# Kernel optimization log

Measured on AMD Instinct MI355X. Metric: run time of the kernel, lower is better.

The kernel has to match this reference:

```python
import jax, jax.numpy as jnp
import numpy as np
import math

B, S, E, H, F, V, L = 2, 2048, 1024, 16, 4096, 32000, 2
D = E // H
START = 1
EPS = 1e-6


def setup_inputs() -> dict:
    key = jax.random.key(0)
    ks = jax.random.split(key, 16)
    k_emb = 1.0 / math.sqrt(V)
    std = 0.02
    inp = {
        "tokens": jax.random.randint(ks[0], (B, S), 0, V),
        "word_embed": jax.random.normal(ks[1], (V, E), jnp.float32) * k_emb,
        "pos_embed": jax.random.normal(ks[2], (S, E), jnp.float32) * k_emb,
        "unembed_b": jnp.zeros((V,), jnp.float32),
        "kqv_w": jax.random.normal(ks[3], (L, 3 * E, E), jnp.float32) * std,
        "wo_w": jax.random.normal(ks[4], (L, E, E), jnp.float32) * std,
        "up_w": jax.random.normal(ks[5], (L, F, E), jnp.float32) * std,
        "up_b": jnp.zeros((L, F), jnp.float32),
        "down_w": jax.random.normal(ks[6], (L, E, F), jnp.float32) * std,
        "down_b": jnp.zeros((L, E), jnp.float32),
        "ln1_s": jnp.ones((L, E), jnp.float32),
        "ln1_b": jnp.zeros((L, E), jnp.float32),
        "ln2_s": jnp.ones((L, E), jnp.float32),
        "ln2_b": jnp.zeros((L, E), jnp.float32),
    }
    return inp


def _layer_norm(x, scale, bias):
    m = jnp.mean(x, axis=-1, keepdims=True)
    v = jnp.var(x, axis=-1, keepdims=True)  # biased, matches torch LayerNorm
    return (x - m) / jnp.sqrt(v + EPS) * scale + bias


def _causal_block_mask(tokens):
    # block-diagonal segments split at START tokens, plus causal triu
    is_start = tokens == START
    seg = jnp.cumsum(is_start, axis=1)  # [B,S]
    block = seg[:, :, None] != seg[:, None, :]  # [B,S,S]
    triu = jnp.triu(jnp.ones((S, S), bool), k=1)
    return triu[None, :, :] | block  # [B,S,S], True = masked


def _resetting_positions(tokens):
    is_start = tokens == START
    is_start = is_start.at[:, 0].set(True)
    pos = jnp.arange(S)
    start_pos = jnp.where(is_start, pos[None, :], 0)
    last_start = jax.lax.cummax(start_pos, axis=1)
    return pos[None, :] - last_start  # [B,S]


def reference(tokens, word_embed, pos_embed, unembed_b, kqv_w, wo_w,
              up_w, up_b, down_w, down_b, ln1_s, ln1_b, ln2_s, ln2_b):
    mask = _causal_block_mask(tokens)[:, None, :, :]  # [B,1,S,S]
    rel_pos = _resetting_positions(tokens)
    x = word_embed[tokens] + pos_embed[rel_pos]  # [B,S,E]
    scale = 1.0 / math.sqrt(D)

    for l in range(L):
        # attention
        qkv = (x @ kqv_w[l].T).reshape(B, S, 3, H, D)
        k, q, v = qkv[:, :, 0], qkv[:, :, 1], qkv[:, :, 2]  # [B,S,H,D]
        attn = jnp.einsum('bqhd,bkhd->bhqk', q, k) * scale
        attn = jnp.where(mask, -jnp.inf, attn)
        attn = jax.nn.softmax(attn, axis=-1)
        out = jnp.einsum('bhqk,bkhd->bqhd', attn, v).reshape(B, S, E)
        out = out @ wo_w[l].T
        x = _layer_norm(out + x, ln1_s[l], ln1_b[l])
        # FFN
        h = jax.nn.relu(x @ up_w[l].T + up_b[l])
        h = h @ down_w[l].T + down_b[l]
        x = _layer_norm(h + x, ln2_s[l], ln2_b[l])

    # weight-tied unembed
    logits = x @ word_embed.T + unembed_b  # [B,S,V]
    return logits
```

## Files before the change

### kernel.cpp

```cpp
#include <hip/hip_runtime.h>
#include <hip/hip_bf16.h>

#define BB 2
#define SS 2048
#define EE 1024
#define HH 16
#define DD 64
#define FF 4096
#define VV 32000
#define LL 2
#define BS (BB*SS)

#define NEG_HUGE (-3.402823466e+38f)
#define SC_LOG2 (0.18033688011112042f)

typedef __attribute__((ext_vector_type(4)))  float  f32x4;
typedef __attribute__((ext_vector_type(16))) float  f32x16;
typedef __attribute__((ext_vector_type(8)))  __bf16 bf16x8;
typedef __attribute__((ext_vector_type(4)))  __bf16 bf16x4;

__device__ inline bf16x8 to_bf8(float4 a, float4 b) {
  bf16x8 r;
  r[0] = (__bf16)a.x; r[1] = (__bf16)a.y; r[2] = (__bf16)a.z; r[3] = (__bf16)a.w;
  r[4] = (__bf16)b.x; r[5] = (__bf16)b.y; r[6] = (__bf16)b.z; r[7] = (__bf16)b.w;
  return r;
}

typedef const unsigned int __attribute__((address_space(1)))* gptr_t;
typedef unsigned int __attribute__((address_space(3)))* lptr_t;
__device__ inline void gload16(const void* g, void* l) {
  __builtin_amdgcn_global_load_lds((gptr_t)g, (lptr_t)l, 16, 0, 0);
}

__global__ __launch_bounds__(1024) void lastart_scan(
    const int* __restrict__ tokens, int* __restrict__ ls) {
  __shared__ int buf[SS];
  const int b = blockIdx.x, t = threadIdx.x;
#pragma unroll
  for (int j = 0; j < 2; ++j) {
    int i = t + j * 1024;
    buf[i] = (i > 0 && tokens[b*SS + i] == 1) ? i : 0;
  }
  __syncthreads();
  for (int off = 1; off < SS; off <<= 1) {
    int i0 = t, i1 = t + 1024;
    int v0 = (i0 >= off) ? max(buf[i0], buf[i0 - off]) : buf[i0];
    int v1 = (i1 >= off) ? max(buf[i1], buf[i1 - off]) : buf[i1];
    __syncthreads();
    buf[i0] = v0; buf[i1] = v1;
    __syncthreads();
  }
#pragma unroll
  for (int j = 0; j < 2; ++j) {
    int i = t + j * 1024;
    ls[b*SS + i] = buf[i];
  }
}

__global__ __launch_bounds__(256) void embed_kernel(
    const int* __restrict__ tokens, const int* __restrict__ ls,
    const float* __restrict__ we, const float* __restrict__ pe,
    float* __restrict__ x, __bf16* __restrict__ xb) {
  int row = blockIdx.x;
  int s = row & (SS - 1);
  int tok = tokens[row];
  int rp = s - ls[row];
  const float4* w4 = (const float4*)(we + (size_t)tok * EE);
  const float4* p4 = (const float4*)(pe + (size_t)rp * EE);
  float4 a = w4[threadIdx.x];
  float4 b = p4[threadIdx.x];
  float4 o; o.x = a.x + b.x; o.y = a.y + b.y; o.z = a.z + b.z; o.w = a.w + b.w;
  ((float4*)(x + (size_t)row * EE))[threadIdx.x] = o;
  bf16x4 ob4;
  ob4[0] = (__bf16)o.x; ob4[1] = (__bf16)o.y; ob4[2] = (__bf16)o.z; ob4[3] = (__bf16)o.w;
  *(bf16x4*)(xb + (size_t)row * EE + threadIdx.x * 4) = ob4;
}

__global__ __launch_bounds__(256) void cvt_bf16_kernel(
    const float* __restrict__ src, __bf16* __restrict__ dst, int n) {
  int i = (blockIdx.x * 256 + threadIdx.x) * 8;
  if (i + 8 > n) return;
  float4 a = *(const float4*)(src + i);
  float4 b = *(const float4*)(src + i + 4);
  *(bf16x8*)(dst + i) = to_bf8(a, b);
}

__device__ inline void stage_half8(const __bf16* __restrict__ base,
                                   __bf16* region, int K, int kofs,
                                   int col8, int srow, int sdst) {
#pragma unroll
  for (int p = 0; p < 2; ++p)
    gload16(base + (size_t)(p * 128 + srow) * K + kofs + col8,
            region + p * 4096 + sdst);
}

template<int NMT, bool BIAS, bool RELU, bool OUTBF16>
__global__ __launch_bounds__(512, 2) void gemm_8ph(
    const __bf16* __restrict__ A, const __bf16* __restrict__ W,
    const float* __restrict__ bias, void* __restrict__ Cv,
    int N, int K, int nmg) {
  __shared__ __bf16 lds[8][8192];
  const int t = threadIdx.x, l = t & 63, w = t >> 6;
  const int nwg = gridDim.x, orig = blockIdx.x;
  const int q = nwg >> 3, r = nwg & 7, xcd = orig & 7, pos = orig >> 3;
  const int wgid = (xcd < r ? xcd*(q+1) : r*(q+1) + (xcd-r)*q) + pos;
  const int mgrp = wgid % nmg, n0 = (wgid / nmg) * 256;
  const int wm = w >> 2, wn = w & 3;
  const int fr = l & 15, c8 = l >> 4;
  const int swz = (c8 ^ ((fr >> 1) & 3)) * 8;
  const int roA = (wm*128 + fr) * 32 + swz;
  const int roB = (wn*64  + fr) * 32 + swz;
  const int col8 = ((t & 3) ^ ((t >> 3) & 3)) * 8;
  const int srow = t >> 2;
  const int sdst = (t >> 6) * 512;

  const __bf16* Wb = W + (size_t)n0 * K;
  const int ng = NMT * 16;

  float bv[4];
#pragma unroll
  for (int j = 0; j < 4; ++j) bv[j] = BIAS ? bias[n0 + wn*64 + fr + j*16] : 0.0f;

  f32x4 acc[8][4] = {};

#define ABASE(g2) (A + (size_t)(mgrp*NMT + ((g2) >> 4)) * 256 * K)
#define KOFS(g2)  (((g2) & 15) * 64)

  stage_half8(ABASE(0), &lds[0][0], K, 0,  col8, srow, sdst);
  stage_half8(Wb,       &lds[2][0], K, 0,  col8, srow, sdst);
  stage_half8(ABASE(0), &lds[1][0], K, 32, col8, srow, sdst);
  stage_half8(Wb,       &lds[3][0], K, 32, col8, srow, sdst);
  stage_half8(ABASE(1), &lds[4][0], K, 64, col8, srow, sdst);
  stage_half8(Wb,       &lds[6][0], K, 64, col8, srow, sdst);
  asm volatile("s_waitcnt vmcnt(4)" ::: "memory");
  __builtin_amdgcn_s_barrier();

  for (int g = 0; g < ng; ++g) {
    const int c = g & 1;
    const int rA = c*4, rB = c*4 + 2;
    bf16x8 afr0[4], afr1[4], bfr[4];
#pragma unroll
    for (int j = 0; j < 4; ++j) bfr[j]  = *(const bf16x8*)&lds[rB][roB + j*512];
#pragma unroll
    for (int i = 0; i < 4; ++i) afr0[i] = *(const bf16x8*)&lds[rA][roA + i*512];
#pragma unroll
    for (int i = 0; i < 4; ++i) afr1[i] = *(const bf16x8*)&lds[rA][roA + (i+4)*512];
    if (g + 1 < ng)
      stage_half8(ABASE(g+1), &lds[(c^1)*4 + 1][0], K, KOFS(g+1) + 32, col8, srow, sdst);
    __builtin_amdgcn_s_barrier();
    __builtin_amdgcn_s_setprio(1);
#pragma unroll
    for (int i = 0; i < 4; ++i)
#pragma unroll
      for (int j = 0; j < 4; ++j)
        acc[i][j] = __builtin_amdgcn_mfma_f32_16x16x32_bf16(afr0[i], bfr[j], acc[i][j], 0, 0, 0);
    __builtin_amdgcn_s_setprio(0);
    __builtin_amdgcn_s_barrier();
    if (g + 1 < ng)
      stage_half8(Wb, &lds[(c^1)*4 + 3][0], K, KOFS(g+1) + 32, col8, srow, sdst);
    __builtin_amdgcn_s_barrier();
    __builtin_amdgcn_s_setprio(1);
#pragma unroll
    for (int i = 0; i < 4; ++i)
#pragma unroll
      for (int j = 0; j < 4; ++j)
        acc[i+4][j] = __builtin_amdgcn_mfma_f32_16x16x32_bf16(afr1[i], bfr[j], acc[i+4][j], 0, 0, 0);
    __builtin_amdgcn_s_setprio(0);
    if (g < ng - 1) { asm volatile("s_waitcnt vmcnt(8)" ::: "memory"); }
    else            { asm volatile("s_waitcnt vmcnt(0)" ::: "memory"); }
    __builtin_amdgcn_s_barrier();
#pragma unroll
    for (int j = 0; j < 4; ++j) bfr[j]  = *(const bf16x8*)&lds[rB + 1][roB + j*512];
#pragma unroll
    for (int i = 0; i < 4; ++i) afr0[i] = *(const bf16x8*)&lds[rA + 1][roA + i*512];
#pragma unroll
    for (int i = 0; i < 4; ++i) afr1[i] = *(const bf16x8*)&lds[rA + 1][roA + (i+4)*512];
    if (g + 2 < ng)
      stage_half8(ABASE(g+2), &lds[c*4][0], K, KOFS(g+2), col8, srow, sdst);
    __builtin_amdgcn_s_barrier();
    __builtin_amdgcn_s_setprio(1);
#pragma unroll
    for (int i = 0; i < 4; ++i)
#pragma unroll
      for (int j = 0; j < 4; ++j)
        acc[i][j] = __builtin_amdgcn_mfma_f32_16x16x32_bf16(afr0[i], bfr[j], acc[i][j], 0, 0, 0);
    __builtin_amdgcn_s_setprio(0);
    __builtin_amdgcn_s_barrier();
    if (g + 2 < ng)
      stage_half8(Wb, &lds[c*4 + 2][0], K, KOFS(g+2), col8, srow, sdst);
    __builtin_amdgcn_s_barrier();
    __builtin_amdgcn_s_setprio(1);
#pragma unroll
    for (int i = 0; i < 4; ++i)
#pragma unroll
      for (int j = 0; j < 4; ++j)
        acc[i+4][j] = __builtin_amdgcn_mfma_f32_16x16x32_bf16(afr1[i], bfr[j], acc[i+4][j], 0, 0, 0);
    __builtin_amdgcn_s_setprio(0);
    if (g < ng - 2)       { asm volatile("s_waitcnt vmcnt(8)" ::: "memory"); }
    else if (g == ng - 2) { asm volatile("s_waitcnt vmcnt(4)" ::: "memory"); }
    __builtin_amdgcn_s_barrier();
    if ((g & 15) == 15) {
      const int orow = (mgrp*NMT + (g >> 4)) * 256 + wm*128 + c8 * 4;
      const int ocol = n0 + wn*64 + fr;
#pragma unroll
      for (int i = 0; i < 8; ++i)
#pragma unroll
        for (int j = 0; j < 4; ++j) {
#pragma unroll
          for (int rr = 0; rr < 4; ++rr) {
            float v = acc[i][j][rr] + bv[j];
            if (RELU) v = fmaxf(v, 0.0f);
            if (OUTBF16)
              ((__bf16*)Cv)[(size_t)(orow + i*16 + rr) * N + ocol + j*16] = (__bf16)v;
            else
              ((float*)Cv)[(size_t)(orow + i*16 + rr) * N + ocol + j*16] = v;
          }
          acc[i][j] = (f32x4){};
        }
    }
  }
#undef ABASE
#undef KOFS
}

template<int T, int BM>
__device__ inline void stage2(const __bf16* __restrict__ Ab,
                              const __bf16* __restrict__ Wb,
                              __bf16* la, __bf16* lb, int K, int k0, int t) {
  const int col8 = (t & 3) ^ ((t >> 3) & 3);
  const int cofs = k0 + col8 * 8;
  const int wbase = (t >> 6) * 512;
#pragma unroll
  for (int p = 0; p < (BM * 32) / (T * 8); ++p) {
    const int row = p * (T >> 2) + (t >> 2);
    gload16(Ab + (size_t)row * K + cofs, la + p * T * 8 + wbase);
    gload16(Wb + (size_t)row * K + cofs, lb + p * T * 8 + wbase);
  }
}

template<int RW, int WM, int WN, bool BIAS, bool RELU, bool OUTBF16>
__global__ __launch_bounds__(WM*WN*64, 2) void gemm_deep(
    const __bf16* __restrict__ A, const __bf16* __restrict__ W,
    const float* __restrict__ bias, void* __restrict__ Cv,
    int N, int K, int nbx) {
  constexpr int T  = WM * WN * 64;
  constexpr int BM = WM * RW * 16;
  __shared__ __bf16 lds[4][2][BM * 32];
  const int t = threadIdx.x, l = t & 63, w = t >> 6;
  const int nwg = gridDim.x, orig = blockIdx.x;
  const int q = nwg >> 3, r = nwg & 7, xcd = orig & 7, pos = orig >> 3;
  const int wgid = (xcd < r ? xcd*(q+1) : r*(q+1) + (xcd-r)*q) + pos;
  const int m0 = (wgid % nbx) * BM, n0 = (wgid / nbx) * BM;
  const int wm = w / WN, wn = w % WN;
  const int fr = l & 15, c8 = l >> 4;
  const int slot = (c8 ^ ((fr >> 1) & 3)) * 8;

  const __bf16* Abase = A + (size_t)m0 * K;
  const __bf16* Wbase = W + (size_t)n0 * K;

  f32x4 acc[RW][4] = {};

  const int nk = K >> 5;
  stage2<T,BM>(Abase, Wbase, &lds[0][0][0], &lds[0][1][0], K, 0,  t);
  stage2<T,BM>(Abase, Wbase, &lds[1][0][0], &lds[1][1][0], K, 32, t);
  stage2<T,BM>(Abase, Wbase, &lds[2][0][0], &lds[2][1][0], K, 64, t);

  for (int kt = 0; kt < nk; ++kt) {
    const int cur = kt & 3;
    if (kt + 3 < nk) {
      const int nb = (kt + 3) & 3;
      stage2<T,BM>(Abase, Wbase, &lds[nb][0][0], &lds[nb][1][0], K, (kt+3)*32, t);
      asm volatile("s_waitcnt vmcnt(8)" ::: "memory");
    } else if (kt + 2 < nk) {
      asm volatile("s_waitcnt vmcnt(8)" ::: "memory");
    } else if (kt + 1 < nk) {
      asm volatile("s_waitcnt vmcnt(4)" ::: "memory");
    } else {
      asm volatile("s_waitcnt vmcnt(0)" ::: "memory");
    }
    __builtin_amdgcn_s_barrier();
    __builtin_amdgcn_sched_barrier(0);
    const __bf16* La = &lds[cur][0][0];
    const __bf16* Lb = &lds[cur][1][0];
    bf16x8 bfr[4];
#pragma unroll
    for (int j = 0; j < 4; ++j)
      bfr[j] = *(const bf16x8*)&Lb[(wn*64 + j*16 + fr) * 32 + slot];
    __builtin_amdgcn_s_setprio(1);
#pragma unroll
    for (int i = 0; i < RW; ++i) {
      bf16x8 af = *(const bf16x8*)&La[(wm*(RW*16) + i*16 + fr) * 32 + slot];
#pragma unroll
      for (int j = 0; j < 4; ++j)
        acc[i][j] = __builtin_amdgcn_mfma_f32_16x16x32_bf16(af, bfr[j], acc[i][j], 0, 0, 0);
    }
    __builtin_amdgcn_s_setprio(0);
    __builtin_amdgcn_sched_barrier(0);
    __builtin_amdgcn_s_barrier();
    __builtin_amdgcn_sched_barrier(0);
  }

  const int orow = m0 + wm*(RW*16) + c8 * 4;
  const int ocol = n0 + wn*64 + fr;
#pragma unroll
  for (int i = 0; i < RW; ++i)
#pragma unroll
    for (int j = 0; j < 4; ++j) {
      const int col = ocol + j * 16;
      const float bv = BIAS ? bias[col] : 0.0f;
#pragma unroll
      for (int rr = 0; rr < 4; ++rr) {
        float v = acc[i][j][rr] + bv;
        if (RELU) v = fmaxf(v, 0.0f);
        if (OUTBF16)
          ((__bf16*)Cv)[(size_t)(orow + i*16 + rr) * N + col] = (__bf16)v;
        else
          ((float*)Cv)[(size_t)(orow + i*16 + rr) * N + col] = v;
      }
    }
}

template<bool WBF16, bool BIAS, bool RELU, bool OUTBF16>
__global__ __launch_bounds__(256) void gemm_fast(
    const __bf16* __restrict__ A, const void* __restrict__ Wv,
    const float* __restrict__ bias, void* __restrict__ Cv, int N, int K) {
  __shared__ __bf16 As[128][32];
  __shared__ __bf16 Bs[128][32];
  const int t = threadIdx.x;
  const int m0 = blockIdx.x * 128, n0 = blockIdx.y * 128;
  const int l = t & 63, w = t >> 6;
  const int wm = (w >> 1) * 64, wn = (w & 1) * 64;
  const int fr = l & 15, fk = (l >> 4) * 8;
  const int crow = l >> 2, ccol = (l & 3) * 8;
  const int wrow = t >> 1, wcol = (t & 1) * 16;

  const __bf16* Wb = (const __bf16*)Wv;
  const float*  Wf = (const float*)Wv;

  f32x4 acc[4][4] = {};

  for (int k0 = 0; k0 < K; k0 += 32) {
    float4 wf0, wf1, wf2, wf3;
    if (!WBF16) {
      const float* wp = Wf + (size_t)(n0 + wrow) * K + k0 + wcol;
      wf0 = *(const float4*)(wp);
      wf1 = *(const float4*)(wp + 4);
      wf2 = *(const float4*)(wp + 8);
      wf3 = *(const float4*)(wp + 12);
    }
    __syncthreads();
#pragma unroll
    for (int i = 0; i < 2; ++i) {
      const int c = 2 * w + i;
      gload16(A + (size_t)(m0 + c*16 + crow) * K + k0 + ccol, (__bf16*)As + c*512);
      if (WBF16)
        gload16(Wb + (size_t)(n0 + c*16 + crow) * K + k0 + ccol, (__bf16*)Bs + c*512);
    }
    if (!WBF16) {
      *(bf16x8*)&Bs[wrow][wcol]     = to_bf8(wf0, wf1);
      *(bf16x8*)&Bs[wrow][wcol + 8] = to_bf8(wf2, wf3);
    }
    __syncthreads();
    bf16x8 af[4], bf[4];
#pragma unroll
    for (int i = 0; i < 4; ++i) af[i] = *(const bf16x8*)&As[wm + i*16 + fr][fk];
#pragma unroll
    for (int j = 0; j < 4; ++j) bf[j] = *(const bf16x8*)&Bs[wn + j*16 + fr][fk];
#pragma unroll
    for (int i = 0; i < 4; ++i)
#pragma unroll
      for (int j = 0; j < 4; ++j)
        acc[i][j] = __builtin_amdgcn_mfma_f32_16x16x32_bf16(af[i], bf[j], acc[i][j], 0, 0, 0);
  }

  const int orow = m0 + wm + (l >> 4) * 4;
  const int ocol = n0 + wn + fr;
#pragma unroll
  for (int i = 0; i < 4; ++i)
#pragma unroll
    for (int j = 0; j < 4; ++j) {
      const int col = ocol + j * 16;
      const float bv = BIAS ? bias[col] : 0.0f;
#pragma unroll
      for (int r = 0; r < 4; ++r) {
        float v = acc[i][j][r] + bv;
        if (RELU) v = fmaxf(v, 0.0f);
        if (OUTBF16)
          ((__bf16*)Cv)[(size_t)(orow + i*16 + r) * N + col] = (__bf16)v;
        else
          ((float*)Cv)[(size_t)(orow + i*16 + r) * N + col] = v;
      }
    }
}

__global__ __launch_bounds__(256) void ln_res_kernel(
    const __bf16* __restrict__ y, float* __restrict__ x, __bf16* __restrict__ xb,
    const float* __restrict__ sc, const float* __restrict__ bs) {
  __shared__ float red[8];
  int row = blockIdx.x, t = threadIdx.x;
  bf16x4 a4 = *(const bf16x4*)(y + (size_t)row * EE + t * 4);
  float4* x4 = (float4*)(x + (size_t)row * EE);
  float4 c = x4[t];
  float v0 = (float)a4[0] + c.x, v1 = (float)a4[1] + c.y;
  float v2 = (float)a4[2] + c.z, v3 = (float)a4[3] + c.w;
  float s = v0 + v1 + v2 + v3;
  float q = v0*v0 + v1*v1 + v2*v2 + v3*v3;
#pragma unroll
  for (int off = 32; off; off >>= 1) {
    s += __shfl_xor(s, off);
    q += __shfl_xor(q, off);
  }
  int w = t >> 6;
  if ((t & 63) == 0) { red[w] = s; red[4 + w] = q; }
  __syncthreads();
  s = red[0] + red[1] + red[2] + red[3];
  q = red[4] + red[5] + red[6] + red[7];
  float mean = s * (1.0f / EE);
  float var  = q * (1.0f / EE) - mean * mean;
  float r = 1.0f / sqrtf(var + 1e-6f);
  float4 ss = ((const float4*)sc)[t];
  float4 bb = ((const float4*)bs)[t];
  float4 o;
  o.x = (v0 - mean) * r * ss.x + bb.x;
  o.y = (v1 - mean) * r * ss.y + bb.y;
  o.z = (v2 - mean) * r * ss.z + bb.z;
  o.w = (v3 - mean) * r * ss.w + bb.w;
  x4[t] = o;
  bf16x4 ob4;
  ob4[0] = (__bf16)o.x; ob4[1] = (__bf16)o.y; ob4[2] = (__bf16)o.z; ob4[3] = (__bf16)o.w;
  *(bf16x4*)(xb + (size_t)row * EE + t * 4) = ob4;
}

__global__ __launch_bounds__(256) void attn_mfma(
    const __bf16* __restrict__ qkv, const int* __restrict__ ls,
    __bf16* __restrict__ out) {
  const int id = blockIdx.x;
  const int z = id >> 8, rem = id & 255;
  const int qt0 = rem & 15, h = rem >> 4, b = z;
  const int qt = z ? (15 - qt0) : qt0;
  __shared__ f32x4 lds4[2304];
  char* lds = (char*)lds4;
  __bf16* Ks = (__bf16*)lds;
  __bf16* Vs = (__bf16*)(lds + 9216);
  __shared__ int redmin[4];
  const int t = threadIdx.x, w = t >> 6, l = t & 63;
  __bf16* Pq = (__bf16*)(lds + 18432 + w * 4608);
  const int r = l & 31, hi = l >> 5;
  const int qb = qt * 128, qw = qb + w * 32, qg = qw + r;
  const int Lq = ls[b*SS + qg];

  {
    int mn = Lq;
#pragma unroll
    for (int off = 1; off < 64; off <<= 1) mn = min(mn, __shfl_xor(mn, off));
    if (l == 0) redmin[w] = mn;
  }

  bf16x8 qf[4];
  {
    const __bf16* qrow = qkv + (size_t)(b*SS + qg) * 3*EE + EE + h*DD + 8*hi;
#pragma unroll
    for (int ds = 0; ds < 4; ++ds) qf[ds] = *(const bf16x8*)(qrow + 16*ds);
  }
  __syncthreads();
  const int ktmin = min(min(redmin[0], redmin[1]), min(redmin[2], redmin[3])) >> 6;
  const int ktmax = 2*qt + 1;

  f32x16 oacc[2] = {};
  float m_r = NEG_HUGE, lsum = 0.0f;

  for (int kt = ktmin; kt <= ktmax; ++kt) {
    __syncthreads();
    {
      const int kr = t >> 2, c0 = (t & 3) * 16;
      const __bf16* kg = qkv + (size_t)(b*SS + kt*64 + kr) * 3*EE + h*DD + c0;
      const __bf16* vg = kg + 2*EE;
      bf16x8 k0 = *(const bf16x8*)kg;
      bf16x8 k1 = *(const bf16x8*)(kg + 8);
      bf16x8 v0 = *(const bf16x8*)vg;
      bf16x8 v1 = *(const bf16x8*)(vg + 8);
      *(bf16x8*)&Ks[kr*72 + c0]     = k0;
      *(bf16x8*)&Ks[kr*72 + c0 + 8] = k1;
      const int vc = (kr + 8*(t & 3)) & 63;
#pragma unroll
      for (int j = 0; j < 8; ++j) {
        Vs[(c0 + j)*72 + vc]     = v0[j];
        Vs[(c0 + 8 + j)*72 + vc] = v1[j];
      }
    }
    __syncthreads();

    bool act0 = (kt*64)      <= (qw + 31);
    bool act1 = (kt*64 + 32) <= (qw + 31);
    if (!act0) continue;

    f32x16 st[2];
    st[0] = (f32x16){};
    st[1] = (f32x16){};
#pragma unroll
    for (int ds = 0; ds < 4; ++ds) {
      bf16x8 kf = *(const bf16x8*)&Ks[(r)*72 + 16*ds + 8*hi];
      st[0] = __builtin_amdgcn_mfma_f32_32x32x16_bf16(kf, qf[ds], st[0], 0, 0, 0);
    }
    if (act1) {
#pragma unroll
      for (int ds = 0; ds < 4; ++ds) {
        bf16x8 kf = *(const bf16x8*)&Ks[(32 + r)*72 + 16*ds + 8*hi];
        st[1] = __builtin_amdgcn_mfma_f32_32x32x16_bf16(kf, qf[ds], st[1], 0, 0, 0);
      }
    }

    float tmax = NEG_HUGE;
#pragma unroll
    for (int kt2 = 0; kt2 < 2; ++kt2) {
#pragma unroll
      for (int reg = 0; reg < 16; ++reg) {
        const int key = kt*64 + 32*kt2 + (reg & 3) + 8*(reg >> 2) + 4*hi;
        float s = (kt2 == 0 || act1) ? st[kt2][reg] * SC_LOG2 : NEG_HUGE;
        const bool valid = (key >= Lq) && (key <= qg);
        s = valid ? s : NEG_HUGE;
        st[kt2][reg] = s;
        tmax = fmaxf(tmax, s);
      }
    }
    tmax = fmaxf(tmax, __shfl_xor(tmax, 32));
    const float m_old = m_r;
    const float m_new = fmaxf(m_r, tmax);
    m_r = m_new;
    const unsigned long long grew = __ballot(m_new != m_old);

    float psum = 0.0f;
#pragma unroll
    for (int kt2 = 0; kt2 < 2; ++kt2) {
#pragma unroll
      for (int g2 = 0; g2 < 4; ++g2) {
        bf16x4 pk;
#pragma unroll
        for (int j = 0; j < 4; ++j) {
          float p = exp2f(st[kt2][g2*4 + j] - m_new);
          psum += p;
          pk[j] = (__bf16)p;
        }
        *(bf16x4*)&Pq[r*72 + 32*kt2 + 8*g2 + 4*hi] = pk;
      }
    }
    psum += __shfl_xor(psum, 32);
    if (grew) {
      const float alpha = exp2f(m_old - m_new);
      lsum = lsum * alpha + psum;
      oacc[0] *= alpha;
      oacc[1] *= alpha;
    } else {
      lsum += psum;
    }

#pragma unroll
    for (int ks = 0; ks < 4; ++ks) {
      if (kt*64 + 16*ks > qw + 31) continue;
      bf16x8 pf = *(const bf16x8*)&Pq[r*72 + 16*ks + 8*hi];
#pragma unroll
      for (int mt = 0; mt < 2; ++mt) {
        const int d = 32*mt + r;
        const int vcol = (16*ks + 8*hi + 8*((d >> 4) & 3)) & 63;
        bf16x8 vf = *(const bf16x8*)&Vs[d*72 + vcol];
        oacc[mt] = __builtin_amdgcn_mfma_f32_32x32x16_bf16(vf, pf, oacc[mt], 0, 0, 0);
      }
    }
  }

  __syncthreads();
  float* Ot = (float*)(lds + w * 8448);
  const float rinv = 1.0f / lsum;
#pragma unroll
  for (int mt = 0; mt < 2; ++mt)
#pragma unroll
    for (int reg = 0; reg < 16; ++reg) {
      const int d = 32*mt + (reg & 3) + 8*(reg >> 2) + 4*hi;
      Ot[d*33 + r] = oacc[mt][reg] * rinv;
    }
  __syncthreads();
  const int qr0 = l >> 4, dc = (l & 15) * 4;
#pragma unroll
  for (int it = 0; it < 8; ++it) {
    const int qr = qr0 + 4*it;
    bf16x4 ov;
    ov[0] = (__bf16)Ot[(dc+0)*33 + qr];
    ov[1] = (__bf16)Ot[(dc+1)*33 + qr];
    ov[2] = (__bf16)Ot[(dc+2)*33 + qr];
    ov[3] = (__bf16)Ot[(dc+3)*33 + qr];
    *(bf16x4*)(out + (size_t)(b*SS + qw + qr) * EE + h*DD + dc) = ov;
  }
}

extern "C" void kernel_launch(void* const* d_in, const int* in_sizes, int n_in,
                              void* d_out, int out_size, void* d_ws, size_t ws_size,
                              hipStream_t stream) {
  const int*   tokens     = (const int*)  d_in[0];
  const float* word_embed = (const float*)d_in[1];
  const float* pos_embed  = (const float*)d_in[2];
  const float* unembed_b  = (const float*)d_in[3];
  const float* kqv_w      = (const float*)d_in[4];
  const float* wo_w       = (const float*)d_in[5];
  const float* up_w       = (const float*)d_in[6];
  const float* up_b       = (const float*)d_in[7];
  const float* down_w     = (const float*)d_in[8];
  const float* down_b     = (const float*)d_in[9];
  const float* ln1_s      = (const float*)d_in[10];
  const float* ln1_b      = (const float*)d_in[11];
  const float* ln2_s      = (const float*)d_in[12];
  const float* ln2_b      = (const float*)d_in[13];
  float* logits = (float*)d_out;

  char* ob = (char*)d_out;
  __bf16* qkv  = (__bf16*)ob;
  __bf16* t0   = (__bf16*)(ob +  24ull*1024*1024);
  __bf16* hbuf = (__bf16*)(ob +  32ull*1024*1024);
  __bf16* ybuf = (__bf16*)(ob +  64ull*1024*1024);
  __bf16* wcvt = (__bf16*)(ob +  80ull*1024*1024);
  float*  x    = (float*) (ob + 131ull*1024*1024);
  __bf16* kqvb  = wcvt;
  __bf16* wob   = kqvb + (size_t)LL*3*EE*EE;
  __bf16* upb   = wob  + (size_t)LL*EE*EE;
  __bf16* downb = upb  + (size_t)LL*FF*EE;
  int*    ls   = (int*)d_ws;
  __bf16* xb   = (__bf16*)((char*)d_ws + 65536);
  __bf16* webf = (__bf16*)((char*)d_ws + 65536 + 8ull*1024*1024);
  const bool bigws = ws_size >= (size_t)(65536 + 8ull*1024*1024 + (size_t)VV*EE*2);

  lastart_scan<<<BB, 1024, 0, stream>>>(tokens, ls);
  embed_kernel<<<BS, 256, 0, stream>>>(tokens, ls, word_embed, pos_embed, x, xb);

  cvt_bf16_kernel<<<LL*3*EE*EE/2048, 256, 0, stream>>>(kqv_w,  kqvb,  LL*3*EE*EE);
  cvt_bf16_kernel<<<LL*EE*EE/2048,   256, 0, stream>>>(wo_w,   wob,   LL*EE*EE);
  cvt_bf16_kernel<<<LL*FF*EE/2048,   256, 0, stream>>>(up_w,   upb,   LL*FF*EE);
  cvt_bf16_kernel<<<LL*EE*FF/2048,   256, 0, stream>>>(down_w, downb, LL*EE*FF);
  if (bigws)
    cvt_bf16_kernel<<<VV*EE/2048, 256, 0, stream>>>(word_embed, webf, VV*EE);

  for (int l = 0; l < LL; ++l) {
    gemm_8ph<1,false,false,true><<<(BS/256)*(3*EE/256), 512, 0, stream>>>(
        xb, kqvb + (size_t)l*3*EE*EE, nullptr, qkv, 3*EE, EE, BS/256);
    attn_mfma<<<512, 256, 0, stream>>>(qkv, ls, t0);
    gemm_deep<4,2,2,false,false,true><<<(BS/128)*(EE/128), 256, 0, stream>>>(
        t0, wob + (size_t)l*EE*EE, nullptr, ybuf, EE, EE, BS/128);
    ln_res_kernel<<<BS, 256, 0, stream>>>(ybuf, x, xb, ln1_s + l*EE, ln1_b + l*EE);
    gemm_8ph<1,true,true,true><<<(BS/256)*(FF/256), 512, 0, stream>>>(
        xb, upb + (size_t)l*FF*EE, up_b + (size_t)l*FF, hbuf, FF, EE, BS/256);
    gemm_deep<4,2,2,true,false,true><<<(BS/128)*(EE/128), 256, 0, stream>>>(
        hbuf, downb + (size_t)l*EE*FF, down_b + (size_t)l*EE, ybuf, EE, FF, BS/128);
    ln_res_kernel<<<BS, 256, 0, stream>>>(ybuf, x, xb, ln2_s + l*EE, ln2_b + l*EE);
  }

  if (bigws) {
    gemm_8ph<8,true,false,false><<<(VV/256)*2, 512, 0, stream>>>(
        xb, webf, unembed_b, logits, VV, EE, 2);
  } else {
    gemm_fast<false,true,false,false><<<dim3(BS/128, VV/128), 256, 0, stream>>>(
        xb, word_embed, unembed_b, logits, VV, EE);
  }
}
```

Measured before the change: 903.9 us.

## Split-K the FFN down-projection GEMM and add a bias-reduce kernel

The down-projection GEMM (K=4096, N=1024) now runs as two K-halves, each written as fp32 partials to a scratch region of the output buffer. A separate kernel sums the two partials, adds the bias and writes bf16. The aim is to double the workgroup count from 256 tiles, so more compute units are busy on this long-K GEMM. In exchange it adds fp32 partial traffic of about 32MB per layer plus an extra kernel launch.

```diff
diff --git a/kernel.cpp b/kernel.cpp
--- a/kernel.cpp
+++ b/kernel.cpp
@@ -83,6 +83,27 @@
   float4 a = *(const float4*)(src + i);
   float4 b = *(const float4*)(src + i + 4);
   *(bf16x8*)(dst + i) = to_bf8(a, b);
+}
+
+__global__ __launch_bounds__(256) void splitk_reduce_bias(
+    const float* __restrict__ p0, const float* __restrict__ p1,
+    const float* __restrict__ bias, __bf16* __restrict__ out, int N) {
+  const int i = (blockIdx.x * 256 + threadIdx.x) * 8;
+  float4 a0 = *(const float4*)(p0 + i);
+  float4 a1 = *(const float4*)(p0 + i + 4);
+  float4 b0 = *(const float4*)(p1 + i);
+  float4 b1 = *(const float4*)(p1 + i + 4);
+  const float* bp = bias + (i & (N - 1));
+  bf16x8 o;
+  o[0] = (__bf16)(a0.x + b0.x + bp[0]);
+  o[1] = (__bf16)(a0.y + b0.y + bp[1]);
+  o[2] = (__bf16)(a0.z + b0.z + bp[2]);
+  o[3] = (__bf16)(a0.w + b0.w + bp[3]);
+  o[4] = (__bf16)(a1.x + b1.x + bp[4]);
+  o[5] = (__bf16)(a1.y + b1.y + bp[5]);
+  o[6] = (__bf16)(a1.z + b1.z + bp[6]);
+  o[7] = (__bf16)(a1.w + b1.w + bp[7]);
+  *(bf16x8*)(out + i) = o;
 }
 
 __device__ inline void stage_half8(const __bf16* __restrict__ base,
@@ -320,6 +341,80 @@
     }
 }
 
+template<int RW, int WM, int WN>
+__global__ __launch_bounds__(WM*WN*64, 2) void gemm_deep_sk(
+    const __bf16* __restrict__ A, const __bf16* __restrict__ W,
+    float* __restrict__ P, int N, int Kfull, int Klen, int nbx, int M) {
+  constexpr int T  = WM * WN * 64;
+  constexpr int BM = WM * RW * 16;
+  __shared__ __bf16 lds[4][2][BM * 32];
+  const int t = threadIdx.x, l = t & 63, w = t >> 6;
+  const int nwg = gridDim.x, orig = blockIdx.x;
+  const int q = nwg >> 3, r = nwg & 7, xcd = orig & 7, pos = orig >> 3;
+  const int wgid = (xcd < r ? xcd*(q+1) : r*(q+1) + (xcd-r)*q) + pos;
+  const int slice = wgid & 1, tile = wgid >> 1;
+  const int m0 = (tile % nbx) * BM, n0 = (tile / nbx) * BM;
+  const int wm = w / WN, wn = w % WN;
+  const int fr = l & 15, c8 = l >> 4;
+  const int slot = (c8 ^ ((fr >> 1) & 3)) * 8;
+
+  const __bf16* Abase = A + (size_t)m0 * Kfull + slice * Klen;
+  const __bf16* Wbase = W + (size_t)n0 * Kfull + slice * Klen;
+  float* Pb = P + (size_t)slice * M * N;
+
+  f32x4 acc[RW][4] = {};
+
+  const int nk = Klen >> 5;
+  stage2<T,BM>(Abase, Wbase, &lds[0][0][0], &lds[0][1][0], Kfull, 0,  t);
+  stage2<T,BM>(Abase, Wbase, &lds[1][0][0], &lds[1][1][0], Kfull, 32, t);
+  stage2<T,BM>(Abase, Wbase, &lds[2][0][0], &lds[2][1][0], Kfull, 64, t);
+
+  for (int kt = 0; kt < nk; ++kt) {
+    const int cur = kt & 3;
+    if (kt + 3 < nk) {
+      const int nb = (kt + 3) & 3;
+      stage2<T,BM>(Abase, Wbase, &lds[nb][0][0], &lds[nb][1][0], Kfull, (kt+3)*32, t);
+      asm volatile("s_waitcnt vmcnt(8)" ::: "memory");
+    } else if (kt + 2 < nk) {
+      asm volatile("s_waitcnt vmcnt(8)" ::: "memory");
+    } else if (kt + 1 < nk) {
+      asm volatile("s_waitcnt vmcnt(4)" ::: "memory");
+    } else {
+      asm volatile("s_waitcnt vmcnt(0)" ::: "memory");
+    }
+    __builtin_amdgcn_s_barrier();
+    __builtin_amdgcn_sched_barrier(0);
+    const __bf16* La = &lds[cur][0][0];
+    const __bf16* Lb = &lds[cur][1][0];
+    bf16x8 bfr[4];
+#pragma unroll
+    for (int j = 0; j < 4; ++j)
+      bfr[j] = *(const bf16x8*)&Lb[(wn*64 + j*16 + fr) * 32 + slot];
+    __builtin_amdgcn_s_setprio(1);
+#pragma unroll
+    for (int i = 0; i < RW; ++i) {
+      bf16x8 af = *(const bf16x8*)&La[(wm*(RW*16) + i*16 + fr) * 32 + slot];
+#pragma unroll
+      for (int j = 0; j < 4; ++j)
+        acc[i][j] = __builtin_amdgcn_mfma_f32_16x16x32_bf16(af, bfr[j], acc[i][j], 0, 0, 0);
+    }
+    __builtin_amdgcn_s_setprio(0);
+    __builtin_amdgcn_sched_barrier(0);
+    __builtin_amdgcn_s_barrier();
+    __builtin_amdgcn_sched_barrier(0);
+  }
+
+  const int orow = m0 + wm*(RW*16) + c8 * 4;
+  const int ocol = n0 + wn*64 + fr;
+#pragma unroll
+  for (int i = 0; i < RW; ++i)
+#pragma unroll
+    for (int j = 0; j < 4; ++j)
+#pragma unroll
+      for (int rr = 0; rr < 4; ++rr)
+        Pb[(size_t)(orow + i*16 + rr) * N + ocol + j*16] = acc[i][j][rr];
+}
+
 template<bool WBF16, bool BIAS, bool RELU, bool OUTBF16>
 __global__ __launch_bounds__(256) void gemm_fast(
     const __bf16* __restrict__ A, const void* __restrict__ Wv,
@@ -618,6 +713,7 @@
   __bf16* ybuf = (__bf16*)(ob +  64ull*1024*1024);
   __bf16* wcvt = (__bf16*)(ob +  80ull*1024*1024);
   float*  x    = (float*) (ob + 131ull*1024*1024);
+  float*  psk  = (float*) (ob + 160ull*1024*1024);
   __bf16* kqvb  = wcvt;
   __bf16* wob   = kqvb + (size_t)LL*3*EE*EE;
   __bf16* upb   = wob  + (size_t)LL*EE*EE;
@@ -646,8 +742,10 @@
     ln_res_kernel<<<BS, 256, 0, stream>>>(ybuf, x, xb, ln1_s + l*EE, ln1_b + l*EE);
     gemm_8ph<1,true,true,true><<<(BS/256)*(FF/256), 512, 0, stream>>>(
         xb, upb + (size_t)l*FF*EE, up_b + (size_t)l*FF, hbuf, FF, EE, BS/256);
-    gemm_deep<4,2,2,true,false,true><<<(BS/128)*(EE/128), 256, 0, stream>>>(
-        hbuf, downb + (size_t)l*EE*FF, down_b + (size_t)l*EE, ybuf, EE, FF, BS/128);
+    gemm_deep_sk<4,2,2><<<2*(BS/128)*(EE/128), 256, 0, stream>>>(
+        hbuf, downb + (size_t)l*EE*FF, psk, EE, FF, FF/2, BS/128, BS);
+    splitk_reduce_bias<<<(BS*EE)/2048, 256, 0, stream>>>(
+        psk, psk + (size_t)BS*EE, down_b + l*EE, ybuf, EE);
     ln_res_kernel<<<BS, 256, 0, stream>>>(ybuf, x, xb, ln2_s + l*EE, ln2_b + l*EE);
   }
 
```

Result: no change. 909.9 us (+0.7%).
